# Optimization experiments

Measured on AMD Instinct MI355X. Metric: run time of the kernel, lower is better.

Reference implementation:

```python
import jax, jax.numpy as jnp
import numpy as np

NUM_BINS = 15
N = 33_554_432  # number of samples


def setup_inputs() -> dict:
    key = jax.random.key(0)
    k1, k2 = jax.random.split(key)
    probs = jax.random.uniform(k1, (N,), dtype=jnp.float32)
    labels = jax.random.randint(k2, (N,), 0, 2, dtype=jnp.int32)
    return {"probs": probs, "labels": labels}


def reference(probs, labels):
    # bins = linspace(0,1,NUM_BINS+1); element falls in bin b iff
    # probs > b/NUM_BINS and probs <= (b+1)/NUM_BINS  =>  b = ceil(p*NUM_BINS)-1.
    n = probs.shape[0]
    idx = jnp.clip(jnp.ceil(probs * NUM_BINS).astype(jnp.int32) - 1, 0, NUM_BINS - 1)
    # elements with probs <= 0 or > 1 fall in no bin (strict lower on bin 0)
    valid = (probs > 0.0) & (probs <= 1.0)
    w = valid.astype(probs.dtype)
    counts = jax.ops.segment_sum(w, idx, num_segments=NUM_BINS)
    sum_conf = jax.ops.segment_sum(probs * w, idx, num_segments=NUM_BINS)
    sum_acc = jax.ops.segment_sum(labels.astype(probs.dtype) * w, idx, num_segments=NUM_BINS)
    denom = jnp.maximum(counts, 1.0)  # safe divide; empty bins contribute 0
    avg_conf = sum_conf / denom
    avg_acc = sum_acc / denom
    ece = jnp.sum((counts / n) * jnp.abs(avg_acc - avg_conf))
    return ece
```

## Files before the change

kernel.cpp:

```cpp
#include <hip/hip_runtime.h>

#define NUM_BINS 15
#define NB 4096
#define NT 256
#define NCOMP 45
#define INV15 0.066666667f

typedef float vfloat4 __attribute__((ext_vector_type(4)));
typedef int   vint4   __attribute__((ext_vector_type(4)));

__device__ __forceinline__ unsigned pack_elem(float pv, int lv, int* bin_out) {
    int bin = (int)ceilf(pv * 15.0f) - 1;
    bin = (min(max(bin, -1), 15)) & 15;
    *bin_out = bin;
    float x = fmaf(pv, 4096.0f, fmaf((float)bin, -4096.0f * INV15, 0.5f));
    unsigned rq = (unsigned)x;
    return ((unsigned)lv << 24) + 0x10000u + rq;
}

struct Batch { vfloat4 p0, p1; vint4 l0, l1; };

__device__ __forceinline__ void load_batch(Batch& b, const vfloat4* __restrict__ p4,
                                           const vint4* __restrict__ l4, int j, int t) {
    const int o = (j << 9) + t;
    b.p0 = __builtin_nontemporal_load(&p4[o]);
    b.p1 = __builtin_nontemporal_load(&p4[o + 256]);
    b.l0 = __builtin_nontemporal_load(&l4[o]);
    b.l1 = __builtin_nontemporal_load(&l4[o + 256]);
}

__device__ __forceinline__ void scatter4(unsigned* histT, vfloat4 p, vint4 l) {
    int b0, b1, b2, b3;
    unsigned k0 = pack_elem(p.x, l.x, &b0);
    unsigned k1 = pack_elem(p.y, l.y, &b1);
    unsigned k2 = pack_elem(p.z, l.z, &b2);
    unsigned k3 = pack_elem(p.w, l.w, &b3);
    atomicAdd(&histT[b0 << 8], k0);
    atomicAdd(&histT[b1 << 8], k1);
    atomicAdd(&histT[b2 << 8], k2);
    atomicAdd(&histT[b3 << 8], k3);
}

__device__ __forceinline__ void consume(const Batch& b, unsigned* histT) {
    scatter4(histT, b.p0, b.l0);
    scatter4(histT, b.p1, b.l1);
}

__global__ __launch_bounds__(NT, 6) void ece_partial(
    const float* __restrict__ probs, const int* __restrict__ labels,
    float* __restrict__ ws, int n4)
{
    __shared__ unsigned hist[16 * NT];
    const int t = threadIdx.x;

    uint4* h4 = (uint4*)hist;
#pragma unroll
    for (int i = 0; i < 4; ++i) h4[i * NT + t] = uint4{0u, 0u, 0u, 0u};
    __syncthreads();

    const int base = blockIdx.x * 2048;
    const vfloat4* __restrict__ p4 = (const vfloat4*)probs + base;
    const vint4*   __restrict__ l4 = (const vint4*)labels + base;
    unsigned* histT = hist + t;

    if (base + 2048 <= n4) {
        Batch A, B;
        load_batch(A, p4, l4, 0, t);
        load_batch(B, p4, l4, 1, t);
        __builtin_amdgcn_sched_barrier(0);
        consume(A, histT);
        load_batch(A, p4, l4, 2, t);
        __builtin_amdgcn_sched_barrier(0);
        consume(B, histT);
        load_batch(B, p4, l4, 3, t);
        __builtin_amdgcn_sched_barrier(0);
        consume(A, histT);
        consume(B, histT);
    } else {
        for (int j = 0; j < 8; ++j) {
            const int idx = (j << 8) + t;
            if (base + idx < n4) {
                vfloat4 p = p4[idx];
                vint4   l = l4[idx];
                scatter4(histT, p, l);
            }
        }
    }
    __syncthreads();

    const int r = t >> 4, s = t & 15;
    float csum = 0.f, asum = 0.f, rsum = 0.f;
#pragma unroll
    for (int k = 0; k < 16; ++k) {
        unsigned v = hist[(r << 8) + (s << 4) + k];
        asum += (float)(v >> 24);
        csum += (float)((v >> 16) & 0xFFu);
        rsum += (float)(v & 0xFFFFu);
    }
#pragma unroll
    for (int o = 8; o; o >>= 1) {
        csum += __shfl_down(csum, o);
        asum += __shfl_down(asum, o);
        rsum += __shfl_down(rsum, o);
    }
    if (s == 0 && r < NUM_BINS) {
        float conf = fmaf(csum, (float)r * INV15, rsum * 2.44140625e-4f);
        ws[r * NB + blockIdx.x]                  = csum;
        ws[(NUM_BINS + r) * NB + blockIdx.x]     = asum;
        ws[(2 * NUM_BINS + r) * NB + blockIdx.x] = conf;
    }
}

__global__ __launch_bounds__(1024) void ece_final(
    const float* __restrict__ ws, float* __restrict__ out, float n)
{
    __shared__ float sums[NCOMP];
    const int wave = threadIdx.x >> 6;
    const int lane = threadIdx.x & 63;

    for (int c = wave; c < NCOMP; c += 16) {
        const float4* row4 = (const float4*)(ws + c * NB);
        float s = 0.f;
#pragma unroll
        for (int k = 0; k < NB / 256; ++k) {
            float4 v = row4[lane + (k << 6)];
            s += (v.x + v.y) + (v.z + v.w);
        }
#pragma unroll
        for (int o = 32; o; o >>= 1) s += __shfl_down(s, o);
        if (lane == 0) sums[c] = s;
    }
    __syncthreads();

    if (threadIdx.x == 0) {
        float ece = 0.f;
#pragma unroll
        for (int b = 0; b < NUM_BINS; ++b) {
            float cnt = sums[b];
            float acc = sums[NUM_BINS + b];
            float cf  = sums[2 * NUM_BINS + b];
            float denom = fmaxf(cnt, 1.f);
            ece += (cnt / n) * fabsf(acc / denom - cf / denom);
        }
        out[0] = ece;
    }
}

extern "C" void kernel_launch(void* const* d_in, const int* in_sizes, int n_in,
                              void* d_out, int out_size, void* d_ws, size_t ws_size,
                              hipStream_t stream)
{
    const float* probs  = (const float*)d_in[0];
    const int*   labels = (const int*)d_in[1];
    const int n = in_sizes[0];

    ece_partial<<<NB, NT, 0, stream>>>(probs, labels, (float*)d_ws, n / 4);
    ece_final<<<1, 1024, 0, stream>>>((const float*)d_ws, (float*)d_out, (float)n);
}
```

Baseline: 259.3 us.

## Fuse partial and final ECE kernels with atomics and last-block reduction

Merges the two-kernel reduction into one kernel. Per-block bin sums are accumulated with global float atomics, and the last block to finish (found via an atomic counter) computes the final ECE. Each block now processes twice as much data with a longer double-buffered load pipeline, and nontemporal loads become regular loads. This removes the second launch and the workspace pass, but adds a memset and contended atomics, and float accumulation order is no longer deterministic.

```diff
diff --git a/kernel.cpp b/kernel.cpp
--- a/kernel.cpp
+++ b/kernel.cpp
@@ -1,9 +1,8 @@
 #include <hip/hip_runtime.h>
 
 #define NUM_BINS 15
-#define NB 4096
+#define NB 2048
 #define NT 256
-#define NCOMP 45
 #define INV15 0.066666667f
 
 typedef float vfloat4 __attribute__((ext_vector_type(4)));
@@ -23,10 +22,10 @@
 __device__ __forceinline__ void load_batch(Batch& b, const vfloat4* __restrict__ p4,
                                            const vint4* __restrict__ l4, int j, int t) {
     const int o = (j << 9) + t;
-    b.p0 = __builtin_nontemporal_load(&p4[o]);
-    b.p1 = __builtin_nontemporal_load(&p4[o + 256]);
-    b.l0 = __builtin_nontemporal_load(&l4[o]);
-    b.l1 = __builtin_nontemporal_load(&l4[o + 256]);
+    b.p0 = p4[o];
+    b.p1 = p4[o + 256];
+    b.l0 = l4[o];
+    b.l1 = l4[o + 256];
 }
 
 __device__ __forceinline__ void scatter4(unsigned* histT, vfloat4 p, vint4 l) {
@@ -46,9 +45,9 @@
     scatter4(histT, b.p1, b.l1);
 }
 
-__global__ __launch_bounds__(NT, 6) void ece_partial(
+__global__ __launch_bounds__(NT, 6) void ece_fused(
     const float* __restrict__ probs, const int* __restrict__ labels,
-    float* __restrict__ ws, int n4)
+    float* __restrict__ ws, float* __restrict__ out, int n4, float inv_n)
 {
     __shared__ unsigned hist[16 * NT];
     const int t = threadIdx.x;
@@ -58,26 +57,32 @@
     for (int i = 0; i < 4; ++i) h4[i * NT + t] = uint4{0u, 0u, 0u, 0u};
     __syncthreads();
 
-    const int base = blockIdx.x * 2048;
+    const int base = blockIdx.x * 4096;
     const vfloat4* __restrict__ p4 = (const vfloat4*)probs + base;
     const vint4*   __restrict__ l4 = (const vint4*)labels + base;
     unsigned* histT = hist + t;
 
-    if (base + 2048 <= n4) {
+    if (base + 4096 <= n4) {
         Batch A, B;
         load_batch(A, p4, l4, 0, t);
         load_batch(B, p4, l4, 1, t);
         __builtin_amdgcn_sched_barrier(0);
-        consume(A, histT);
-        load_batch(A, p4, l4, 2, t);
+        consume(A, histT); load_batch(A, p4, l4, 2, t);
         __builtin_amdgcn_sched_barrier(0);
-        consume(B, histT);
-        load_batch(B, p4, l4, 3, t);
+        consume(B, histT); load_batch(B, p4, l4, 3, t);
+        __builtin_amdgcn_sched_barrier(0);
+        consume(A, histT); load_batch(A, p4, l4, 4, t);
+        __builtin_amdgcn_sched_barrier(0);
+        consume(B, histT); load_batch(B, p4, l4, 5, t);
+        __builtin_amdgcn_sched_barrier(0);
+        consume(A, histT); load_batch(A, p4, l4, 6, t);
+        __builtin_amdgcn_sched_barrier(0);
+        consume(B, histT); load_batch(B, p4, l4, 7, t);
         __builtin_amdgcn_sched_barrier(0);
         consume(A, histT);
         consume(B, histT);
     } else {
-        for (int j = 0; j < 8; ++j) {
+        for (int j = 0; j < 16; ++j) {
             const int idx = (j << 8) + t;
             if (base + idx < n4) {
                 vfloat4 p = p4[idx];
@@ -105,44 +110,34 @@
     }
     if (s == 0 && r < NUM_BINS) {
         float conf = fmaf(csum, (float)r * INV15, rsum * 2.44140625e-4f);
-        ws[r * NB + blockIdx.x]                  = csum;
-        ws[(NUM_BINS + r) * NB + blockIdx.x]     = asum;
-        ws[(2 * NUM_BINS + r) * NB + blockIdx.x] = conf;
+        atomicAdd(&ws[r], csum);
+        atomicAdd(&ws[NUM_BINS + r], asum);
+        atomicAdd(&ws[2 * NUM_BINS + r], conf);
     }
-}
 
-__global__ __launch_bounds__(1024) void ece_final(
-    const float* __restrict__ ws, float* __restrict__ out, float n)
-{
-    __shared__ float sums[NCOMP];
-    const int wave = threadIdx.x >> 6;
-    const int lane = threadIdx.x & 63;
-
-    for (int c = wave; c < NCOMP; c += 16) {
-        const float4* row4 = (const float4*)(ws + c * NB);
-        float s = 0.f;
-#pragma unroll
-        for (int k = 0; k < NB / 256; ++k) {
-            float4 v = row4[lane + (k << 6)];
-            s += (v.x + v.y) + (v.z + v.w);
-        }
-#pragma unroll
-        for (int o = 32; o; o >>= 1) s += __shfl_down(s, o);
-        if (lane == 0) sums[c] = s;
+    __syncthreads();
+    if (t == 0) {
+        __threadfence();
+        unsigned* ctr = (unsigned*)ws + 48;
+        unsigned old = atomicAdd(ctr, 1u);
+        hist[0] = (old == NB - 1) ? 1u : 0u;
     }
     __syncthreads();
 
-    if (threadIdx.x == 0) {
-        float ece = 0.f;
+    if (hist[0]) {
+        float term = 0.f;
+        if (t < NUM_BINS) {
+            float c  = atomicAdd(&ws[t], 0.f);
+            float a  = atomicAdd(&ws[NUM_BINS + t], 0.f);
+            float cf = atomicAdd(&ws[2 * NUM_BINS + t], 0.f);
+            float denom = fmaxf(c, 1.f);
+            term = (c * inv_n) * fabsf(a / denom - cf / denom);
+        }
+        if (t < 64) {
 #pragma unroll
-        for (int b = 0; b < NUM_BINS; ++b) {
-            float cnt = sums[b];
-            float acc = sums[NUM_BINS + b];
-            float cf  = sums[2 * NUM_BINS + b];
-            float denom = fmaxf(cnt, 1.f);
-            ece += (cnt / n) * fabsf(acc / denom - cf / denom);
+            for (int o = 8; o; o >>= 1) term += __shfl_down(term, o);
+            if (t == 0) out[0] = term;
         }
-        out[0] = ece;
     }
 }
 
@@ -154,6 +149,7 @@
     const int*   labels = (const int*)d_in[1];
     const int n = in_sizes[0];
 
-    ece_partial<<<NB, NT, 0, stream>>>(probs, labels, (float*)d_ws, n / 4);
-    ece_final<<<1, 1024, 0, stream>>>((const float*)d_ws, (float*)d_out, (float)n);
+    hipMemsetAsync(d_ws, 0, 256, stream);
+    ece_fused<<<NB, NT, 0, stream>>>(probs, labels, (float*)d_ws, (float*)d_out,
+                                     n / 4, 1.0f / (float)n);
 }
```

After: 405.6 us. +56.4%, slower.

## Deepen load pipeline with asm loads, larger batches and explicit vmcnt waits

Applied to the files above, without the earlier changes.

Each block now handles 16384 elements instead of 8192, and the block count drops to 2048. Batches grow from 4 to 8 dwordx4 loads per thread. Loads are issued with inline-asm global_load_dwordx4 using a scalar base plus a vector offset, and explicit s_waitcnt vmcnt(8)/vmcnt(0) waits let the next batch stay in flight while the current one is scattered into the LDS histogram. The goal is more outstanding memory traffic per wave and less address arithmetic. In exchange the nontemporal hint is dropped, register pressure rises and the grid has fewer blocks to cover latency; the packed 8-bit count field still fits the 64 elements each thread now handles.

```diff
diff --git a/kernel.cpp b/kernel.cpp
--- a/kernel.cpp
+++ b/kernel.cpp
@@ -1,7 +1,7 @@
 #include <hip/hip_runtime.h>
 
 #define NUM_BINS 15
-#define NB 4096
+#define NB 2048
 #define NT 256
 #define NCOMP 45
 #define INV15 0.066666667f
@@ -18,16 +18,37 @@
     return ((unsigned)lv << 24) + 0x10000u + rq;
 }
 
-struct Batch { vfloat4 p0, p1; vint4 l0, l1; };
+__device__ __forceinline__ vfloat4 gload_f4(const float* base, unsigned voff) {
+    vfloat4 r;
+    asm volatile("global_load_dwordx4 %0, %1, %2"
+                 : "=v"(r) : "v"(voff), "s"(base) : "memory");
+    return r;
+}
+__device__ __forceinline__ vint4 gload_i4(const int* base, unsigned voff) {
+    vint4 r;
+    asm volatile("global_load_dwordx4 %0, %1, %2"
+                 : "=v"(r) : "v"(voff), "s"(base) : "memory");
+    return r;
+}
 
-__device__ __forceinline__ void load_batch(Batch& b, const vfloat4* __restrict__ p4,
-                                           const vint4* __restrict__ l4, int j, int t) {
-    const int o = (j << 9) + t;
-    b.p0 = __builtin_nontemporal_load(&p4[o]);
-    b.p1 = __builtin_nontemporal_load(&p4[o + 256]);
-    b.l0 = __builtin_nontemporal_load(&l4[o]);
-    b.l1 = __builtin_nontemporal_load(&l4[o + 256]);
+struct Batch { vfloat4 p0, p1, p2, p3; vint4 l0, l1, l2, l3; };
+
+__device__ __forceinline__ void load_batch(Batch& b, const float* __restrict__ p,
+                                           const int* __restrict__ l, unsigned voff) {
+    b.p0 = gload_f4(p,        voff);
+    b.p1 = gload_f4(p + 1024, voff);
+    b.p2 = gload_f4(p + 2048, voff);
+    b.p3 = gload_f4(p + 3072, voff);
+    b.l0 = gload_i4(l,        voff);
+    b.l1 = gload_i4(l + 1024, voff);
+    b.l2 = gload_i4(l + 2048, voff);
+    b.l3 = gload_i4(l + 3072, voff);
 }
+
+#define WAIT_VM8()  do { asm volatile("s_waitcnt vmcnt(8)" ::: "memory"); \
+                         __builtin_amdgcn_sched_barrier(0); } while (0)
+#define WAIT_VM0()  do { asm volatile("s_waitcnt vmcnt(0)" ::: "memory"); \
+                         __builtin_amdgcn_sched_barrier(0); } while (0)
 
 __device__ __forceinline__ void scatter4(unsigned* histT, vfloat4 p, vint4 l) {
     int b0, b1, b2, b3;
@@ -44,11 +65,13 @@
 __device__ __forceinline__ void consume(const Batch& b, unsigned* histT) {
     scatter4(histT, b.p0, b.l0);
     scatter4(histT, b.p1, b.l1);
+    scatter4(histT, b.p2, b.l2);
+    scatter4(histT, b.p3, b.l3);
 }
 
 __global__ __launch_bounds__(NT, 6) void ece_partial(
     const float* __restrict__ probs, const int* __restrict__ labels,
-    float* __restrict__ ws, int n4)
+    float* __restrict__ ws, int n)
 {
     __shared__ unsigned hist[16 * NT];
     const int t = threadIdx.x;
@@ -58,28 +81,32 @@
     for (int i = 0; i < 4; ++i) h4[i * NT + t] = uint4{0u, 0u, 0u, 0u};
     __syncthreads();
 
-    const int base = blockIdx.x * 2048;
-    const vfloat4* __restrict__ p4 = (const vfloat4*)probs + base;
-    const vint4*   __restrict__ l4 = (const vint4*)labels + base;
+    const int base = blockIdx.x * 16384;
+    const float* __restrict__ p_blk = probs + base;
+    const int*   __restrict__ l_blk = labels + base;
     unsigned* histT = hist + t;
+    const unsigned t16 = (unsigned)t << 4;
 
-    if (base + 2048 <= n4) {
+    if (base + 16384 <= n) {
         Batch A, B;
-        load_batch(A, p4, l4, 0, t);
-        load_batch(B, p4, l4, 1, t);
-        __builtin_amdgcn_sched_barrier(0);
+        load_batch(A, p_blk, l_blk, t16);
+        load_batch(B, p_blk, l_blk, t16 + 16384u);
+        WAIT_VM8();
         consume(A, histT);
-        load_batch(A, p4, l4, 2, t);
-        __builtin_amdgcn_sched_barrier(0);
+        load_batch(A, p_blk, l_blk, t16 + 32768u);
+        WAIT_VM8();
         consume(B, histT);
-        load_batch(B, p4, l4, 3, t);
-        __builtin_amdgcn_sched_barrier(0);
+        load_batch(B, p_blk, l_blk, t16 + 49152u);
+        WAIT_VM8();
         consume(A, histT);
+        WAIT_VM0();
         consume(B, histT);
     } else {
-        for (int j = 0; j < 8; ++j) {
+        const vfloat4* __restrict__ p4 = (const vfloat4*)p_blk;
+        const vint4*   __restrict__ l4 = (const vint4*)l_blk;
+        for (int j = 0; j < 16; ++j) {
             const int idx = (j << 8) + t;
-            if (base + idx < n4) {
+            if (base + idx * 4 < n) {
                 vfloat4 p = p4[idx];
                 vint4   l = l4[idx];
                 scatter4(histT, p, l);
@@ -154,6 +181,6 @@
     const int*   labels = (const int*)d_in[1];
     const int n = in_sizes[0];
 
-    ece_partial<<<NB, NT, 0, stream>>>(probs, labels, (float*)d_ws, n / 4);
+    ece_partial<<<NB, NT, 0, stream>>>(probs, labels, (float*)d_ws, n);
     ece_final<<<1, 1024, 0, stream>>>((const float*)d_ws, (float*)d_out, (float)n);
 }
```

New measurement: 283.6 us. +9.3%, slower.

## Stream inputs through LDS with async global_load_lds in a 4-deep pipeline

Applied to the files above, without the earlier changes.

Replaces the register-held double-buffered loads with async global-to-LDS loads into a 4-slot staging ring. Each wave issues loads for batch j+4 while consuming batch j, using explicit vmcnt waits. Each block now covers 16384 elements, with half as many blocks and a smaller per-thread histogram of 128 slots per bin shared by two threads. The aim is deeper memory-level parallelism and lower register pressure. The cost is more LDS use, which lowers occupancy, and possible atomic contention on the shared histogram slots.

```diff
diff --git a/kernel.cpp b/kernel.cpp
--- a/kernel.cpp
+++ b/kernel.cpp
@@ -1,13 +1,18 @@
 #include <hip/hip_runtime.h>
 
 #define NUM_BINS 15
-#define NB 4096
+#define NB 2048
 #define NT 256
 #define NCOMP 45
 #define INV15 0.066666667f
+#define DEPTH 4
+#define NBATCH 16
 
 typedef float vfloat4 __attribute__((ext_vector_type(4)));
 typedef int   vint4   __attribute__((ext_vector_type(4)));
+
+typedef const __attribute__((address_space(1))) void* gas_ptr;
+typedef __attribute__((address_space(3))) void*       las_ptr;
 
 __device__ __forceinline__ unsigned pack_elem(float pv, int lv, int* bin_out) {
     int bin = (int)ceilf(pv * 15.0f) - 1;
@@ -18,68 +23,80 @@
     return ((unsigned)lv << 24) + 0x10000u + rq;
 }
 
-struct Batch { vfloat4 p0, p1; vint4 l0, l1; };
-
-__device__ __forceinline__ void load_batch(Batch& b, const vfloat4* __restrict__ p4,
-                                           const vint4* __restrict__ l4, int j, int t) {
-    const int o = (j << 9) + t;
-    b.p0 = __builtin_nontemporal_load(&p4[o]);
-    b.p1 = __builtin_nontemporal_load(&p4[o + 256]);
-    b.l0 = __builtin_nontemporal_load(&l4[o]);
-    b.l1 = __builtin_nontemporal_load(&l4[o + 256]);
-}
-
 __device__ __forceinline__ void scatter4(unsigned* histT, vfloat4 p, vint4 l) {
     int b0, b1, b2, b3;
     unsigned k0 = pack_elem(p.x, l.x, &b0);
     unsigned k1 = pack_elem(p.y, l.y, &b1);
     unsigned k2 = pack_elem(p.z, l.z, &b2);
     unsigned k3 = pack_elem(p.w, l.w, &b3);
-    atomicAdd(&histT[b0 << 8], k0);
-    atomicAdd(&histT[b1 << 8], k1);
-    atomicAdd(&histT[b2 << 8], k2);
-    atomicAdd(&histT[b3 << 8], k3);
+    atomicAdd(&histT[b0 << 7], k0);
+    atomicAdd(&histT[b1 << 7], k1);
+    atomicAdd(&histT[b2 << 7], k2);
+    atomicAdd(&histT[b3 << 7], k3);
 }
 
-__device__ __forceinline__ void consume(const Batch& b, unsigned* histT) {
-    scatter4(histT, b.p0, b.l0);
-    scatter4(histT, b.p1, b.l1);
-}
+#define WAITV(N) do { asm volatile("s_waitcnt vmcnt(" #N ")" ::: "memory"); \
+                      __builtin_amdgcn_sched_barrier(0); } while (0)
 
-__global__ __launch_bounds__(NT, 6) void ece_partial(
+__global__ __launch_bounds__(NT, 4) void ece_partial(
     const float* __restrict__ probs, const int* __restrict__ labels,
-    float* __restrict__ ws, int n4)
+    float* __restrict__ ws, int n)
 {
-    __shared__ unsigned hist[16 * NT];
+    __shared__ unsigned hist[16 * 128];
+    __shared__ unsigned stage[DEPTH * 2048];
     const int t = threadIdx.x;
 
     uint4* h4 = (uint4*)hist;
-#pragma unroll
-    for (int i = 0; i < 4; ++i) h4[i * NT + t] = uint4{0u, 0u, 0u, 0u};
+    h4[t]       = uint4{0u, 0u, 0u, 0u};
+    h4[t + 256] = uint4{0u, 0u, 0u, 0u};
     __syncthreads();
 
-    const int base = blockIdx.x * 2048;
-    const vfloat4* __restrict__ p4 = (const vfloat4*)probs + base;
-    const vint4*   __restrict__ l4 = (const vint4*)labels + base;
-    unsigned* histT = hist + t;
+    const int base = blockIdx.x * 16384;
+    const float* __restrict__ p_blk = probs + base;
+    const int*   __restrict__ l_blk = labels + base;
+    unsigned* histT = hist + (t & 127);
+    const int wbase = (t >> 6) << 8;
 
-    if (base + 2048 <= n4) {
-        Batch A, B;
-        load_batch(A, p4, l4, 0, t);
-        load_batch(B, p4, l4, 1, t);
-        __builtin_amdgcn_sched_barrier(0);
-        consume(A, histT);
-        load_batch(A, p4, l4, 2, t);
-        __builtin_amdgcn_sched_barrier(0);
-        consume(B, histT);
-        load_batch(B, p4, l4, 3, t);
-        __builtin_amdgcn_sched_barrier(0);
-        consume(A, histT);
-        consume(B, histT);
+#define ISSUE(j) do {                                                          \
+        __builtin_amdgcn_global_load_lds(                                      \
+            (gas_ptr)(p_blk + (j) * 1024 + t * 4),                             \
+            (las_ptr)&stage[(((j) & (DEPTH - 1)) << 11) + wbase], 16, 0, 0);   \
+        __builtin_amdgcn_global_load_lds(                                      \
+            (gas_ptr)(l_blk + (j) * 1024 + t * 4),                             \
+            (las_ptr)&stage[(((j) & (DEPTH - 1)) << 11) + 1024 + wbase], 16, 0, 0); \
+    } while (0)
+
+#define CONSUME(j) do {                                                        \
+        const int slot = ((j) & (DEPTH - 1)) << 11;                            \
+        vfloat4 p = *(const vfloat4*)&stage[slot + t * 4];                     \
+        vint4   l = *(const vint4*)&stage[slot + 1024 + t * 4];                \
+        scatter4(histT, p, l);                                                 \
+    } while (0)
+
+    if (base + 16384 <= n) {
+        ISSUE(0); ISSUE(1); ISSUE(2); ISSUE(3);
+        WAITV(6); CONSUME(0);  ISSUE(4);
+        WAITV(6); CONSUME(1);  ISSUE(5);
+        WAITV(6); CONSUME(2);  ISSUE(6);
+        WAITV(6); CONSUME(3);  ISSUE(7);
+        WAITV(6); CONSUME(4);  ISSUE(8);
+        WAITV(6); CONSUME(5);  ISSUE(9);
+        WAITV(6); CONSUME(6);  ISSUE(10);
+        WAITV(6); CONSUME(7);  ISSUE(11);
+        WAITV(6); CONSUME(8);  ISSUE(12);
+        WAITV(6); CONSUME(9);  ISSUE(13);
+        WAITV(6); CONSUME(10); ISSUE(14);
+        WAITV(6); CONSUME(11); ISSUE(15);
+        WAITV(6); CONSUME(12);
+        WAITV(4); CONSUME(13);
+        WAITV(2); CONSUME(14);
+        WAITV(0); CONSUME(15);
     } else {
-        for (int j = 0; j < 8; ++j) {
+        const vfloat4* __restrict__ p4 = (const vfloat4*)p_blk;
+        const vint4*   __restrict__ l4 = (const vint4*)l_blk;
+        for (int j = 0; j < 16; ++j) {
             const int idx = (j << 8) + t;
-            if (base + idx < n4) {
+            if (base + idx * 4 < n) {
                 vfloat4 p = p4[idx];
                 vint4   l = l4[idx];
                 scatter4(histT, p, l);
@@ -91,8 +108,8 @@
     const int r = t >> 4, s = t & 15;
     float csum = 0.f, asum = 0.f, rsum = 0.f;
 #pragma unroll
-    for (int k = 0; k < 16; ++k) {
-        unsigned v = hist[(r << 8) + (s << 4) + k];
+    for (int k = 0; k < 8; ++k) {
+        unsigned v = hist[(r << 7) + (s << 3) + k];
         asum += (float)(v >> 24);
         csum += (float)((v >> 16) & 0xFFu);
         rsum += (float)(v & 0xFFFFu);
@@ -154,6 +171,6 @@
     const int*   labels = (const int*)d_in[1];
     const int n = in_sizes[0];
 
-    ece_partial<<<NB, NT, 0, stream>>>(probs, labels, (float*)d_ws, n / 4);
+    ece_partial<<<NB, NT, 0, stream>>>(probs, labels, (float*)d_ws, n);
     ece_final<<<1, 1024, 0, stream>>>((const float*)d_ws, (float*)d_out, (float)n);
 }
```

Measured after the change: 282.9 us. +9.1%, slower.
